# Performance work log

Measured on AMD Instinct MI355X. Metric: run time of the kernel, lower is better.

The kernel has to match this reference:

```python
import jax, jax.numpy as jnp
import numpy as np

N_NODES = 100000
N_EDGES = 3200000
D_FEAT = 256
FILTERS = 256


def setup_inputs() -> dict:
    key = jax.random.key(0)
    k1, k2, k3, k4, k5 = jax.random.split(key, 5)
    x = jax.random.normal(k1, (N_NODES, D_FEAT), dtype=jnp.float32)
    edge_row = jax.random.randint(k2, (N_EDGES,), 0, N_NODES, dtype=jnp.int32)
    edge_col = jax.random.randint(k3, (N_EDGES,), 0, N_NODES, dtype=jnp.int32)
    edge_vals = jnp.ones((N_EDGES,), dtype=jnp.float32)
    w = jax.random.normal(k4, (D_FEAT, FILTERS), dtype=jnp.float32) * (2.0 / D_FEAT) ** 0.5  # he_normal
    b = jax.random.normal(k5, (FILTERS,), dtype=jnp.float32) * 0.05
    return {"x": x, "edge_row": edge_row, "edge_col": edge_col,
            "edge_vals": edge_vals, "w": w, "b": b}


def reference(x, edge_row, edge_col, edge_vals, w, b):
    n = x.shape[0]
    # normalize_A: D = rowsum(A); L = D^{-1/2} A D^{-1/2}
    deg = jax.ops.segment_sum(edge_vals, edge_row, num_segments=n)
    dinv = jnp.where(deg > 0, deg ** -0.5, 0.0)  # [N]
    norm_vals = edge_vals * dinv[edge_row] * dinv[edge_col]  # [E]
    # dense projection then sparse aggregation + bias + relu
    h = x @ w  # [N, F]
    msg = norm_vals[:, None] * h[edge_col]  # [E, F] gather + scale
    agg = jax.ops.segment_sum(msg, edge_row, num_segments=n)  # [N, F]
    return jax.nn.relu(agg + b)
```

## Files before the change

kernel.cpp:

```cpp
#include <hip/hip_runtime.h>
#include <hip/hip_bf16.h>


#define DF   256
#define RSH  7
#define RPB  128
#define CAP  4800
#define CHUNK 8192

typedef __attribute__((ext_vector_type(8))) short short8;
typedef __attribute__((ext_vector_type(4))) float f32x4;

__device__ __forceinline__ unsigned short f2bf(float f) {
    unsigned int u = __float_as_uint(f);
    unsigned int r = (u + 0x7fffu + ((u >> 16) & 1u)) >> 16;
    return (unsigned short)r;
}
__device__ __forceinline__ unsigned int pack2(float a, float b) {
    return (unsigned)f2bf(a) | ((unsigned)f2bf(b) << 16);
}
__device__ __forceinline__ float bflo(unsigned int u) { return __uint_as_float(u << 16); }
__device__ __forceinline__ float bfhi(unsigned int u) { return __uint_as_float(u & 0xffff0000u); }

__global__ __launch_bounds__(256) void bhist_kernel(const int* __restrict__ row,
                                                    int* __restrict__ blockhist, int NB, int E) {
    __shared__ int hist[1024];
    int t = threadIdx.x;
    for (int i = t; i < NB; i += 256) hist[i] = 0;
    __syncthreads();
    int base = blockIdx.x * CHUNK;
    int end = base + CHUNK; if (end > E) end = E;
    for (int i = base + t; i < end; i += 256)
        atomicAdd(&hist[row[i] >> RSH], 1);
    __syncthreads();
    for (int i = t; i < NB; i += 256)
        blockhist[(size_t)blockIdx.x * NB + i] = hist[i];
}

__global__ __launch_bounds__(256) void bscan_kernel(int* __restrict__ blockhist,
                                                    int* __restrict__ buckettot, int NB, int NBLK) {
    __shared__ int ps[256];
    int b = blockIdx.x, t = threadIdx.x;
    int e0 = 2 * t, e1 = 2 * t + 1;
    int v0 = (e0 < NBLK) ? blockhist[(size_t)e0 * NB + b] : 0;
    int v1 = (e1 < NBLK) ? blockhist[(size_t)e1 * NB + b] : 0;
    int tsum = v0 + v1;
    ps[t] = tsum;
    __syncthreads();
    for (int off = 1; off < 256; off <<= 1) {
        int v = (t >= off) ? ps[t - off] : 0;
        __syncthreads();
        ps[t] += v;
        __syncthreads();
    }
    int pre = ps[t] - tsum;
    if (e0 < NBLK) blockhist[(size_t)e0 * NB + b] = pre;
    if (e1 < NBLK) blockhist[(size_t)e1 * NB + b] = pre + v0;
    if (t == 255) buckettot[b] = ps[255];
}

__global__ __launch_bounds__(1024) void btot_kernel(const int* __restrict__ buckettot,
                                                    int* __restrict__ bucket_base, int NB) {
    __shared__ int ps[1024];
    int t = threadIdx.x;
    int v = (t < NB) ? buckettot[t] : 0;
    ps[t] = v;
    __syncthreads();
    for (int off = 1; off < 1024; off <<= 1) {
        int u = (t >= off) ? ps[t - off] : 0;
        __syncthreads();
        ps[t] += u;
        __syncthreads();
    }
    if (t < NB) bucket_base[t] = ps[t] - v;
    if (t == 1023) bucket_base[NB] = ps[1023];
}

__global__ __launch_bounds__(256) void bscatter_kernel(const int* __restrict__ row,
                                                       const int* __restrict__ col,
                                                       const float* __restrict__ vals,
                                                       const int* __restrict__ blockhist,
                                                       const int* __restrict__ bucket_base,
                                                       int2* __restrict__ bedge, int NB, int E) {
    __shared__ int loff[1024];
    int t = threadIdx.x, blk = blockIdx.x;
    for (int i = t; i < NB; i += 256)
        loff[i] = bucket_base[i] + blockhist[(size_t)blk * NB + i];
    __syncthreads();
    int base = blk * CHUNK;
    int end = base + CHUNK; if (end > E) end = E;
    for (int i = base + t; i < end; i += 256) {
        int r = row[i];
        int p = atomicAdd(&loff[r >> RSH], 1);
        bedge[p] = make_int2(((r & (RPB - 1)) << 17) | col[i], __float_as_int(vals[i]));
    }
}

__global__ __launch_bounds__(256) void deg_kernel(const int2* __restrict__ bedge,
                                                  const int* __restrict__ bucket_base,
                                                  float* __restrict__ dinv, int N) {
    __shared__ float acc[RPB];
    int b = blockIdx.x, t = threadIdx.x;
    if (t < RPB) acc[t] = 0.f;
    __syncthreads();
    int s = bucket_base[b], e = bucket_base[b + 1];
    for (int i = s + t; i < e; i += 256) {
        int2 ed = bedge[i];
        atomicAdd(&acc[ed.x >> 17], __int_as_float(ed.y));
    }
    __syncthreads();
    if (t < RPB) {
        int r = b * RPB + t;
        if (r < N) {
            float d = acc[t];
            dinv[r] = (d > 0.f) ? (1.0f / sqrtf(d)) : 0.f;
        }
    }
}

__global__ __launch_bounds__(256) void transpose_kernel(const float* __restrict__ w,
                                                        float* __restrict__ wT) {
    __shared__ float tile[32][33];
    int bx = blockIdx.x * 32, by = blockIdx.y * 32;
    int tx = threadIdx.x, ty = threadIdx.y;
    for (int j = ty; j < 32; j += 8) tile[j][tx] = w[(by + j) * DF + bx + tx];
    __syncthreads();
    for (int j = ty; j < 32; j += 8) wT[(bx + j) * DF + by + tx] = tile[tx][j];
}

__global__ __launch_bounds__(256) void gemm_kernel(const float* __restrict__ x,
                                                   const float* __restrict__ wT,
                                                   const float* __restrict__ dinv,
                                                   unsigned short* __restrict__ h, int N) {
    __shared__ unsigned short Al[128 * 32];
    __shared__ unsigned short Bl[128 * 32];
    int tid = threadIdx.x;
    int by = blockIdx.x, bx = blockIdx.y;
    int wv = tid >> 6, lane = tid & 63;
    int wr = wv >> 1, wc = wv & 1;
    int q = lane >> 4, mi = lane & 15;

    f32x4 acc[4][4];
#pragma unroll
    for (int i = 0; i < 4; ++i)
#pragma unroll
        for (int j = 0; j < 4; ++j) acc[i][j] = (f32x4){0.f, 0.f, 0.f, 0.f};

    int srow = tid >> 1;
    int sseg = (tid & 1) * 16;
    int axrow = by * 128 + srow; if (axrow >= N) axrow = N - 1;
    const float* ax = x + (long)axrow * DF + sseg;
    const float* bxp = wT + (long)(bx * 128 + srow) * DF + sseg;
    unsigned short* Aw = &Al[srow * 32 + sseg];
    unsigned short* Bw = &Bl[srow * 32 + sseg];

    for (int kk = 0; kk < DF; kk += 32) {
        float4 a0 = *(const float4*)(ax + kk);
        float4 a1 = *(const float4*)(ax + kk + 4);
        float4 a2 = *(const float4*)(ax + kk + 8);
        float4 a3 = *(const float4*)(ax + kk + 12);
        float4 b0 = *(const float4*)(bxp + kk);
        float4 b1 = *(const float4*)(bxp + kk + 4);
        float4 b2 = *(const float4*)(bxp + kk + 8);
        float4 b3 = *(const float4*)(bxp + kk + 12);
        __syncthreads();
        uint4 pa, pb;
        pa.x = pack2(a0.x, a0.y); pa.y = pack2(a0.z, a0.w);
        pa.z = pack2(a1.x, a1.y); pa.w = pack2(a1.z, a1.w);
        *(uint4*)Aw = pa;
        pa.x = pack2(a2.x, a2.y); pa.y = pack2(a2.z, a2.w);
        pa.z = pack2(a3.x, a3.y); pa.w = pack2(a3.z, a3.w);
        *(uint4*)(Aw + 8) = pa;
        pb.x = pack2(b0.x, b0.y); pb.y = pack2(b0.z, b0.w);
        pb.z = pack2(b1.x, b1.y); pb.w = pack2(b1.z, b1.w);
        *(uint4*)Bw = pb;
        pb.x = pack2(b2.x, b2.y); pb.y = pack2(b2.z, b2.w);
        pb.z = pack2(b3.x, b3.y); pb.w = pack2(b3.z, b3.w);
        *(uint4*)(Bw + 8) = pb;
        __syncthreads();

        short8 af[4], bf[4];
#pragma unroll
        for (int i = 0; i < 4; ++i)
            af[i] = *(const short8*)&Al[(wr * 64 + i * 16 + mi) * 32 + q * 8];
#pragma unroll
        for (int j = 0; j < 4; ++j)
            bf[j] = *(const short8*)&Bl[(wc * 64 + j * 16 + mi) * 32 + q * 8];
#pragma unroll
        for (int i = 0; i < 4; ++i)
#pragma unroll
            for (int j = 0; j < 4; ++j)
                acc[i][j] = __builtin_amdgcn_mfma_f32_16x16x32_bf16(af[i], bf[j], acc[i][j], 0, 0, 0);
    }

#pragma unroll
    for (int i = 0; i < 4; ++i) {
        int base_row = by * 128 + wr * 64 + i * 16 + q * 4;
#pragma unroll
        for (int r = 0; r < 4; ++r) {
            int rg = base_row + r;
            if (rg < N) {
                float dv = dinv[rg];
#pragma unroll
                for (int j = 0; j < 4; ++j) {
                    int cg = bx * 128 + wc * 64 + j * 16 + mi;
                    h[(long)rg * DF + cg] = f2bf(dv * acc[i][j][r]);
                }
            }
        }
    }
}

__global__ __launch_bounds__(256) void aggb_kernel(const unsigned short* __restrict__ h,
                                                   const int2* __restrict__ bedge,
                                                   const int* __restrict__ bucket_base,
                                                   const float* __restrict__ dinv,
                                                   const float* __restrict__ bias,
                                                   float* __restrict__ out, int N) {
    __shared__ int2 ledge[CAP];
    __shared__ int cnt[RPB];
    __shared__ int lrs[RPB + 1];
    __shared__ int lfill[RPB];
    int b = blockIdx.x, t = threadIdx.x;
    int s = bucket_base[b], e = bucket_base[b + 1];
    int tot = e - s;
    int cap_end = s + (tot < CAP ? tot : CAP);
    if (t < RPB) { cnt[t] = 0; lfill[t] = 0; }
    __syncthreads();
    for (int i = s + t; i < cap_end; i += 256)
        atomicAdd(&cnt[bedge[i].x >> 17], 1);
    __syncthreads();
    int myc = 0;
    if (t < RPB) { myc = cnt[t]; lrs[t] = myc; }
    __syncthreads();
    for (int off = 1; off < RPB; off <<= 1) {
        int v = (t < RPB && t >= off) ? lrs[t - off] : 0;
        __syncthreads();
        if (t < RPB) lrs[t] += v;
        __syncthreads();
    }
    if (t < RPB) {
        int iv = lrs[t];
        lrs[t] = iv - myc;
        if (t == RPB - 1) lrs[RPB] = iv;
    }
    __syncthreads();
    for (int i = s + t; i < cap_end; i += 256) {
        int2 ed = bedge[i];
        int rl = ed.x >> 17;
        int p = lrs[rl] + atomicAdd(&lfill[rl], 1);
        ledge[p] = make_int2(ed.x & 0x1FFFF, ed.y);
    }
    __syncthreads();
    int wv = t >> 6, lane = t & 63;
    int half = lane >> 5;
    int fl = (lane & 31) * 8;
    const unsigned short* hp = h + fl;
    for (int lr = wv; lr < RPB; lr += 4) {
        int r = b * RPB + lr;
        if (r >= N) break;
        int rs = lrs[lr], re = lrs[lr + 1];
        float a0 = 0, a1 = 0, a2 = 0, a3 = 0, a4 = 0, a5 = 0, a6 = 0, a7 = 0;
        int i = rs + half;
        for (; i + 6 < re; i += 8) {
            int2 e0 = ledge[i], e1 = ledge[i + 2], e2 = ledge[i + 4], e3 = ledge[i + 6];
            uint4 u0 = *(const uint4*)(hp + (long)e0.x * DF);
            uint4 u1 = *(const uint4*)(hp + (long)e1.x * DF);
            uint4 u2 = *(const uint4*)(hp + (long)e2.x * DF);
            uint4 u3 = *(const uint4*)(hp + (long)e3.x * DF);
            float v0 = __int_as_float(e0.y), v1 = __int_as_float(e1.y);
            float v2 = __int_as_float(e2.y), v3 = __int_as_float(e3.y);
            a0 += v0 * bflo(u0.x) + v1 * bflo(u1.x) + v2 * bflo(u2.x) + v3 * bflo(u3.x);
            a1 += v0 * bfhi(u0.x) + v1 * bfhi(u1.x) + v2 * bfhi(u2.x) + v3 * bfhi(u3.x);
            a2 += v0 * bflo(u0.y) + v1 * bflo(u1.y) + v2 * bflo(u2.y) + v3 * bflo(u3.y);
            a3 += v0 * bfhi(u0.y) + v1 * bfhi(u1.y) + v2 * bfhi(u2.y) + v3 * bfhi(u3.y);
            a4 += v0 * bflo(u0.z) + v1 * bflo(u1.z) + v2 * bflo(u2.z) + v3 * bflo(u3.z);
            a5 += v0 * bfhi(u0.z) + v1 * bfhi(u1.z) + v2 * bfhi(u2.z) + v3 * bfhi(u3.z);
            a6 += v0 * bflo(u0.w) + v1 * bflo(u1.w) + v2 * bflo(u2.w) + v3 * bflo(u3.w);
            a7 += v0 * bfhi(u0.w) + v1 * bfhi(u1.w) + v2 * bfhi(u2.w) + v3 * bfhi(u3.w);
        }
        for (; i < re; i += 2) {
            int2 e0 = ledge[i];
            float v0 = __int_as_float(e0.y);
            uint4 u0 = *(const uint4*)(hp + (long)e0.x * DF);
            a0 += v0 * bflo(u0.x); a1 += v0 * bfhi(u0.x);
            a2 += v0 * bflo(u0.y); a3 += v0 * bfhi(u0.y);
            a4 += v0 * bflo(u0.z); a5 += v0 * bfhi(u0.z);
            a6 += v0 * bflo(u0.w); a7 += v0 * bfhi(u0.w);
        }
        for (int j = cap_end + half; j < e; j += 2) {
            int2 ed = bedge[j];
            if ((ed.x >> 17) == lr) {
                float v0 = __int_as_float(ed.y);
                uint4 u0 = *(const uint4*)(hp + (long)(ed.x & 0x1FFFF) * DF);
                a0 += v0 * bflo(u0.x); a1 += v0 * bfhi(u0.x);
                a2 += v0 * bflo(u0.y); a3 += v0 * bfhi(u0.y);
                a4 += v0 * bflo(u0.z); a5 += v0 * bfhi(u0.z);
                a6 += v0 * bflo(u0.w); a7 += v0 * bfhi(u0.w);
            }
        }
        a0 += __shfl_xor(a0, 32); a1 += __shfl_xor(a1, 32);
        a2 += __shfl_xor(a2, 32); a3 += __shfl_xor(a3, 32);
        a4 += __shfl_xor(a4, 32); a5 += __shfl_xor(a5, 32);
        a6 += __shfl_xor(a6, 32); a7 += __shfl_xor(a7, 32);
        if (half == 0) {
            float dr = dinv[r];
            float4 b0 = *(const float4*)(bias + fl);
            float4 b1 = *(const float4*)(bias + fl + 4);
            float4 o0, o1;
            o0.x = fmaxf(fmaf(dr, a0, b0.x), 0.f);
            o0.y = fmaxf(fmaf(dr, a1, b0.y), 0.f);
            o0.z = fmaxf(fmaf(dr, a2, b0.z), 0.f);
            o0.w = fmaxf(fmaf(dr, a3, b0.w), 0.f);
            o1.x = fmaxf(fmaf(dr, a4, b1.x), 0.f);
            o1.y = fmaxf(fmaf(dr, a5, b1.y), 0.f);
            o1.z = fmaxf(fmaf(dr, a6, b1.z), 0.f);
            o1.w = fmaxf(fmaf(dr, a7, b1.w), 0.f);
            *(float4*)(out + (long)r * DF + fl) = o0;
            *(float4*)(out + (long)r * DF + fl + 4) = o1;
        }
    }
}

extern "C" void kernel_launch(void* const* d_in, const int* in_sizes, int n_in,
                              void* d_out, int out_size, void* d_ws, size_t ws_size,
                              hipStream_t stream) {
    const float* x   = (const float*)d_in[0];
    const int* erow  = (const int*)d_in[1];
    const int* ecol  = (const int*)d_in[2];
    const float* ev  = (const float*)d_in[3];
    const float* w   = (const float*)d_in[4];
    const float* b   = (const float*)d_in[5];
    float* out = (float*)d_out;

    int N = in_sizes[0] / DF;
    int E = in_sizes[1];
    int NB = (N + RPB - 1) >> RSH;
    int NBLK = (E + CHUNK - 1) / CHUNK;

    char* ws = (char*)d_ws;
    size_t Ea8 = (((size_t)E * 8) + 255) & ~(size_t)255;
    size_t Hs  = (((size_t)N * DF * 2) + 255) & ~(size_t)255;
    size_t Na  = (((size_t)N * 4) + 255) & ~(size_t)255;

    int2* bedge = (int2*)ws;
    char* reg2 = ws + Ea8;
    unsigned short* h = (unsigned short*)reg2;
    int* blockhist = (int*)reg2;
    char* reg3 = reg2 + Hs;
    float* wT = (float*)reg3;
    float* dinv = (float*)(reg3 + 262144);
    int* buckettot = (int*)(reg3 + 262144 + Na);
    int* bucket_base = (int*)(reg3 + 262144 + Na + 8192);

    bhist_kernel<<<NBLK, 256, 0, stream>>>(erow, blockhist, NB, E);
    bscan_kernel<<<NB, 256, 0, stream>>>(blockhist, buckettot, NB, NBLK);
    btot_kernel<<<1, 1024, 0, stream>>>(buckettot, bucket_base, NB);
    bscatter_kernel<<<NBLK, 256, 0, stream>>>(erow, ecol, ev, blockhist, bucket_base, bedge, NB, E);
    deg_kernel<<<NB, 256, 0, stream>>>(bedge, bucket_base, dinv, N);
    transpose_kernel<<<dim3(8, 8), dim3(32, 8), 0, stream>>>(w, wT);
    gemm_kernel<<<dim3((N + 127) / 128, DF / 128), 256, 0, stream>>>(x, wT, dinv, h, N);
    aggb_kernel<<<NB, 256, 0, stream>>>(h, bedge, bucket_base, dinv, b, out, N);
}
```

Measured before the change: 595.0 us.

## Sort edges by row in degree pass, widen GEMM tile, transpose block histogram

The degree kernel becomes a resort kernel. It counts and sums edges per row, then writes each bucket's edges back in row-sorted order, so the aggregation kernel only binary-searches row starts instead of redoing the counting sort. The GEMM now computes all 256 output columns per block, which drops the second grid column and halves re-reading of x. It also pads the LDS stride to reduce bank conflicts and sets an occupancy hint. The block histogram is stored transposed so the scan reads coalesced, at the cost of a second histogram buffer, more GEMM registers and an extra global write pass over the edges.

```diff
diff --git a/kernel.cpp b/kernel.cpp
--- a/kernel.cpp
+++ b/kernel.cpp
@@ -7,6 +7,7 @@
 #define RPB  128
 #define CAP  4800
 #define CHUNK 8192
+#define LSTR 40
 
 typedef __attribute__((ext_vector_type(8))) short short8;
 typedef __attribute__((ext_vector_type(4))) float f32x4;
@@ -23,7 +24,7 @@
 __device__ __forceinline__ float bfhi(unsigned int u) { return __uint_as_float(u & 0xffff0000u); }
 
 __global__ __launch_bounds__(256) void bhist_kernel(const int* __restrict__ row,
-                                                    int* __restrict__ blockhist, int NB, int E) {
+                                                    int* __restrict__ bh1, int NB, int NBLK, int E) {
     __shared__ int hist[1024];
     int t = threadIdx.x;
     for (int i = t; i < NB; i += 256) hist[i] = 0;
@@ -34,16 +35,17 @@
         atomicAdd(&hist[row[i] >> RSH], 1);
     __syncthreads();
     for (int i = t; i < NB; i += 256)
-        blockhist[(size_t)blockIdx.x * NB + i] = hist[i];
-}
-
-__global__ __launch_bounds__(256) void bscan_kernel(int* __restrict__ blockhist,
+        bh1[(size_t)i * NBLK + blockIdx.x] = hist[i];
+}
+
+__global__ __launch_bounds__(256) void bscan_kernel(const int* __restrict__ bh1,
+                                                    int* __restrict__ bh2,
                                                     int* __restrict__ buckettot, int NB, int NBLK) {
     __shared__ int ps[256];
     int b = blockIdx.x, t = threadIdx.x;
     int e0 = 2 * t, e1 = 2 * t + 1;
-    int v0 = (e0 < NBLK) ? blockhist[(size_t)e0 * NB + b] : 0;
-    int v1 = (e1 < NBLK) ? blockhist[(size_t)e1 * NB + b] : 0;
+    int v0 = (e0 < NBLK) ? bh1[(size_t)b * NBLK + e0] : 0;
+    int v1 = (e1 < NBLK) ? bh1[(size_t)b * NBLK + e1] : 0;
     int tsum = v0 + v1;
     ps[t] = tsum;
     __syncthreads();
@@ -54,8 +56,8 @@
         __syncthreads();
     }
     int pre = ps[t] - tsum;
-    if (e0 < NBLK) blockhist[(size_t)e0 * NB + b] = pre;
-    if (e1 < NBLK) blockhist[(size_t)e1 * NB + b] = pre + v0;
+    if (e0 < NBLK) bh2[(size_t)e0 * NB + b] = pre;
+    if (e1 < NBLK) bh2[(size_t)e1 * NB + b] = pre + v0;
     if (t == 255) buckettot[b] = ps[255];
 }
 
@@ -79,13 +81,13 @@
 __global__ __launch_bounds__(256) void bscatter_kernel(const int* __restrict__ row,
                                                        const int* __restrict__ col,
                                                        const float* __restrict__ vals,
-                                                       const int* __restrict__ blockhist,
+                                                       const int* __restrict__ bh2,
                                                        const int* __restrict__ bucket_base,
                                                        int2* __restrict__ bedge, int NB, int E) {
     __shared__ int loff[1024];
     int t = threadIdx.x, blk = blockIdx.x;
     for (int i = t; i < NB; i += 256)
-        loff[i] = bucket_base[i] + blockhist[(size_t)blk * NB + i];
+        loff[i] = bucket_base[i] + bh2[(size_t)blk * NB + i];
     __syncthreads();
     int base = blk * CHUNK;
     int end = base + CHUNK; if (end > E) end = E;
@@ -96,25 +98,69 @@
     }
 }
 
-__global__ __launch_bounds__(256) void deg_kernel(const int2* __restrict__ bedge,
-                                                  const int* __restrict__ bucket_base,
-                                                  float* __restrict__ dinv, int N) {
-    __shared__ float acc[RPB];
+__global__ __launch_bounds__(256) void resort_kernel(int2* __restrict__ bedge,
+                                                     const int* __restrict__ bucket_base,
+                                                     float* __restrict__ dinv, int N) {
+    __shared__ int2 ledge[CAP];
+    __shared__ int cnt[RPB];
+    __shared__ float facc[RPB];
+    __shared__ int lrs[RPB];
+    __shared__ int lfill[RPB];
     int b = blockIdx.x, t = threadIdx.x;
-    if (t < RPB) acc[t] = 0.f;
-    __syncthreads();
     int s = bucket_base[b], e = bucket_base[b + 1];
-    for (int i = s + t; i < e; i += 256) {
-        int2 ed = bedge[i];
-        atomicAdd(&acc[ed.x >> 17], __int_as_float(ed.y));
-    }
-    __syncthreads();
+    int tot = e - s;
+    int ncap = tot < CAP ? tot : CAP;
+    if (t < RPB) { cnt[t] = 0; facc[t] = 0.f; lfill[t] = 0; }
+    for (int i = t; i < ncap; i += 256) ledge[i] = bedge[s + i];
+    int2 ov[8]; int nov = 0;
+#pragma unroll
+    for (int k = 0; k < 8; ++k) {
+        int idx = CAP + t + k * 256;
+        if (idx < tot) { ov[k] = bedge[s + idx]; nov = k + 1; }
+    }
+    __syncthreads();
+    for (int i = t; i < ncap; i += 256) {
+        int2 ed = ledge[i];
+        int rl = ed.x >> 17;
+        atomicAdd(&cnt[rl], 1);
+        atomicAdd(&facc[rl], __int_as_float(ed.y));
+    }
+#pragma unroll
+    for (int k = 0; k < 8; ++k) if (k < nov) {
+        int rl = ov[k].x >> 17;
+        atomicAdd(&cnt[rl], 1);
+        atomicAdd(&facc[rl], __int_as_float(ov[k].y));
+    }
+    __syncthreads();
+    int myc = 0;
+    if (t < RPB) { myc = cnt[t]; lrs[t] = myc; }
+    __syncthreads();
+    for (int off = 1; off < RPB; off <<= 1) {
+        int v = (t < RPB && t >= off) ? lrs[t - off] : 0;
+        __syncthreads();
+        if (t < RPB) lrs[t] += v;
+        __syncthreads();
+    }
+    if (t < RPB) lrs[t] -= myc;
     if (t < RPB) {
         int r = b * RPB + t;
         if (r < N) {
-            float d = acc[t];
+            float d = facc[t];
             dinv[r] = (d > 0.f) ? (1.0f / sqrtf(d)) : 0.f;
         }
+    }
+    __syncthreads();
+    for (int i = t; i < ncap; i += 256) {
+        int2 ed = ledge[i];
+        int rl = ed.x >> 17;
+        int p = atomicAdd(&lfill[rl], 1);
+        bedge[s + lrs[rl] + p] = ed;
+    }
+#pragma unroll
+    for (int k = 0; k < 8; ++k) if (k < nov) {
+        int rl = ov[k].x >> 17;
+        int p = atomicAdd(&lfill[rl], 1);
+        bedge[s + lrs[rl] + p] = ov[k];
     }
 }
 
@@ -128,31 +174,31 @@
     for (int j = ty; j < 32; j += 8) wT[(bx + j) * DF + by + tx] = tile[tx][j];
 }
 
-__global__ __launch_bounds__(256) void gemm_kernel(const float* __restrict__ x,
-                                                   const float* __restrict__ wT,
-                                                   const float* __restrict__ dinv,
-                                                   unsigned short* __restrict__ h, int N) {
-    __shared__ unsigned short Al[128 * 32];
-    __shared__ unsigned short Bl[128 * 32];
+__global__ __launch_bounds__(256, 2) void gemm_kernel(const float* __restrict__ x,
+                                                      const float* __restrict__ wT,
+                                                      const float* __restrict__ dinv,
+                                                      unsigned short* __restrict__ h, int N) {
+    __shared__ unsigned short Al[128 * LSTR];
+    __shared__ unsigned short Bl[256 * LSTR];
     int tid = threadIdx.x;
-    int by = blockIdx.x, bx = blockIdx.y;
+    int by = blockIdx.x;
     int wv = tid >> 6, lane = tid & 63;
     int wr = wv >> 1, wc = wv & 1;
     int q = lane >> 4, mi = lane & 15;
 
-    f32x4 acc[4][4];
+    f32x4 acc[4][8];
 #pragma unroll
     for (int i = 0; i < 4; ++i)
 #pragma unroll
-        for (int j = 0; j < 4; ++j) acc[i][j] = (f32x4){0.f, 0.f, 0.f, 0.f};
+        for (int j = 0; j < 8; ++j) acc[i][j] = (f32x4){0.f, 0.f, 0.f, 0.f};
 
     int srow = tid >> 1;
     int sseg = (tid & 1) * 16;
     int axrow = by * 128 + srow; if (axrow >= N) axrow = N - 1;
     const float* ax = x + (long)axrow * DF + sseg;
-    const float* bxp = wT + (long)(bx * 128 + srow) * DF + sseg;
-    unsigned short* Aw = &Al[srow * 32 + sseg];
-    unsigned short* Bw = &Bl[srow * 32 + sseg];
+    const float* bxp = wT + (long)tid * DF;
+    unsigned short* Aw = &Al[srow * LSTR + sseg];
+    unsigned short* Bw = &Bl[tid * LSTR];
 
     for (int kk = 0; kk < DF; kk += 32) {
         float4 a0 = *(const float4*)(ax + kk);
@@ -163,34 +209,44 @@
         float4 b1 = *(const float4*)(bxp + kk + 4);
         float4 b2 = *(const float4*)(bxp + kk + 8);
         float4 b3 = *(const float4*)(bxp + kk + 12);
-        __syncthreads();
-        uint4 pa, pb;
+        float4 b4 = *(const float4*)(bxp + kk + 16);
+        float4 b5 = *(const float4*)(bxp + kk + 20);
+        float4 b6 = *(const float4*)(bxp + kk + 24);
+        float4 b7 = *(const float4*)(bxp + kk + 28);
+        __syncthreads();
+        uint4 pa;
         pa.x = pack2(a0.x, a0.y); pa.y = pack2(a0.z, a0.w);
         pa.z = pack2(a1.x, a1.y); pa.w = pack2(a1.z, a1.w);
         *(uint4*)Aw = pa;
         pa.x = pack2(a2.x, a2.y); pa.y = pack2(a2.z, a2.w);
         pa.z = pack2(a3.x, a3.y); pa.w = pack2(a3.z, a3.w);
         *(uint4*)(Aw + 8) = pa;
+        uint4 pb;
         pb.x = pack2(b0.x, b0.y); pb.y = pack2(b0.z, b0.w);
         pb.z = pack2(b1.x, b1.y); pb.w = pack2(b1.z, b1.w);
         *(uint4*)Bw = pb;
         pb.x = pack2(b2.x, b2.y); pb.y = pack2(b2.z, b2.w);
         pb.z = pack2(b3.x, b3.y); pb.w = pack2(b3.z, b3.w);
         *(uint4*)(Bw + 8) = pb;
-        __syncthreads();
-
-        short8 af[4], bf[4];
+        pb.x = pack2(b4.x, b4.y); pb.y = pack2(b4.z, b4.w);
+        pb.z = pack2(b5.x, b5.y); pb.w = pack2(b5.z, b5.w);
+        *(uint4*)(Bw + 16) = pb;
+        pb.x = pack2(b6.x, b6.y); pb.y = pack2(b6.z, b6.w);
+        pb.z = pack2(b7.x, b7.y); pb.w = pack2(b7.z, b7.w);
+        *(uint4*)(Bw + 24) = pb;
+        __syncthreads();
+
+        short8 af[4];
 #pragma unroll
         for (int i = 0; i < 4; ++i)
-            af[i] = *(const short8*)&Al[(wr * 64 + i * 16 + mi) * 32 + q * 8];
-#pragma unroll
-        for (int j = 0; j < 4; ++j)
-            bf[j] = *(const short8*)&Bl[(wc * 64 + j * 16 + mi) * 32 + q * 8];
-#pragma unroll
-        for (int i = 0; i < 4; ++i)
-#pragma unroll
-            for (int j = 0; j < 4; ++j)
-                acc[i][j] = __builtin_amdgcn_mfma_f32_16x16x32_bf16(af[i], bf[j], acc[i][j], 0, 0, 0);
+            af[i] = *(const short8*)&Al[(wr * 64 + i * 16 + mi) * LSTR + q * 8];
+#pragma unroll
+        for (int j = 0; j < 8; ++j) {
+            short8 bfj = *(const short8*)&Bl[(wc * 128 + j * 16 + mi) * LSTR + q * 8];
+#pragma unroll
+            for (int i = 0; i < 4; ++i)
+                acc[i][j] = __builtin_amdgcn_mfma_f32_16x16x32_bf16(af[i], bfj, acc[i][j], 0, 0, 0);
+        }
     }
 
 #pragma unroll
@@ -202,8 +258,8 @@
             if (rg < N) {
                 float dv = dinv[rg];
 #pragma unroll
-                for (int j = 0; j < 4; ++j) {
-                    int cg = bx * 128 + wc * 64 + j * 16 + mi;
+                for (int j = 0; j < 8; ++j) {
+                    int cg = wc * 128 + j * 16 + mi;
                     h[(long)rg * DF + cg] = f2bf(dv * acc[i][j][r]);
                 }
             }
@@ -218,38 +274,20 @@
                                                    const float* __restrict__ bias,
                                                    float* __restrict__ out, int N) {
     __shared__ int2 ledge[CAP];
-    __shared__ int cnt[RPB];
     __shared__ int lrs[RPB + 1];
-    __shared__ int lfill[RPB];
     int b = blockIdx.x, t = threadIdx.x;
     int s = bucket_base[b], e = bucket_base[b + 1];
     int tot = e - s;
-    int cap_end = s + (tot < CAP ? tot : CAP);
-    if (t < RPB) { cnt[t] = 0; lfill[t] = 0; }
-    __syncthreads();
-    for (int i = s + t; i < cap_end; i += 256)
-        atomicAdd(&cnt[bedge[i].x >> 17], 1);
-    __syncthreads();
-    int myc = 0;
-    if (t < RPB) { myc = cnt[t]; lrs[t] = myc; }
-    __syncthreads();
-    for (int off = 1; off < RPB; off <<= 1) {
-        int v = (t < RPB && t >= off) ? lrs[t - off] : 0;
-        __syncthreads();
-        if (t < RPB) lrs[t] += v;
-        __syncthreads();
-    }
-    if (t < RPB) {
-        int iv = lrs[t];
-        lrs[t] = iv - myc;
-        if (t == RPB - 1) lrs[RPB] = iv;
-    }
-    __syncthreads();
-    for (int i = s + t; i < cap_end; i += 256) {
-        int2 ed = bedge[i];
-        int rl = ed.x >> 17;
-        int p = lrs[rl] + atomicAdd(&lfill[rl], 1);
-        ledge[p] = make_int2(ed.x & 0x1FFFF, ed.y);
+    int ncap = tot < CAP ? tot : CAP;
+    for (int i = t; i < ncap; i += 256) ledge[i] = bedge[s + i];
+    __syncthreads();
+    if (t < RPB + 1) {
+        int lo = 0, hi = ncap;
+        while (lo < hi) {
+            int m = (lo + hi) >> 1;
+            if ((ledge[m].x >> 17) < t) lo = m + 1; else hi = m;
+        }
+        lrs[t] = lo;
     }
     __syncthreads();
     int wv = t >> 6, lane = t & 63;
@@ -264,10 +302,10 @@
         int i = rs + half;
         for (; i + 6 < re; i += 8) {
             int2 e0 = ledge[i], e1 = ledge[i + 2], e2 = ledge[i + 4], e3 = ledge[i + 6];
-            uint4 u0 = *(const uint4*)(hp + (long)e0.x * DF);
-            uint4 u1 = *(const uint4*)(hp + (long)e1.x * DF);
-            uint4 u2 = *(const uint4*)(hp + (long)e2.x * DF);
-            uint4 u3 = *(const uint4*)(hp + (long)e3.x * DF);
+            uint4 u0 = *(const uint4*)(hp + (long)(e0.x & 0x1FFFF) * DF);
+            uint4 u1 = *(const uint4*)(hp + (long)(e1.x & 0x1FFFF) * DF);
+            uint4 u2 = *(const uint4*)(hp + (long)(e2.x & 0x1FFFF) * DF);
+            uint4 u3 = *(const uint4*)(hp + (long)(e3.x & 0x1FFFF) * DF);
             float v0 = __int_as_float(e0.y), v1 = __int_as_float(e1.y);
             float v2 = __int_as_float(e2.y), v3 = __int_as_float(e3.y);
             a0 += v0 * bflo(u0.x) + v1 * bflo(u1.x) + v2 * bflo(u2.x) + v3 * bflo(u3.x);
@@ -279,18 +317,19 @@
             a6 += v0 * bflo(u0.w) + v1 * bflo(u1.w) + v2 * bflo(u2.w) + v3 * bflo(u3.w);
             a7 += v0 * bfhi(u0.w) + v1 * bfhi(u1.w) + v2 * bfhi(u2.w) + v3 * bfhi(u3.w);
         }
-        for (; i < re; i += 2) {
+        for (; i < re && i < ncap; i += 2) {
             int2 e0 = ledge[i];
             float v0 = __int_as_float(e0.y);
-            uint4 u0 = *(const uint4*)(hp + (long)e0.x * DF);
+            uint4 u0 = *(const uint4*)(hp + (long)(e0.x & 0x1FFFF) * DF);
             a0 += v0 * bflo(u0.x); a1 += v0 * bfhi(u0.x);
             a2 += v0 * bflo(u0.y); a3 += v0 * bfhi(u0.y);
             a4 += v0 * bflo(u0.z); a5 += v0 * bfhi(u0.z);
             a6 += v0 * bflo(u0.w); a7 += v0 * bfhi(u0.w);
         }
-        for (int j = cap_end + half; j < e; j += 2) {
-            int2 ed = bedge[j];
-            if ((ed.x >> 17) == lr) {
+        if (tot > CAP && re > CAP) {
+            int j2 = (rs > CAP ? rs : CAP) + half;
+            for (; j2 < re; j2 += 2) {
+                int2 ed = bedge[s + j2];
                 float v0 = __int_as_float(ed.y);
                 uint4 u0 = *(const uint4*)(hp + (long)(ed.x & 0x1FFFF) * DF);
                 a0 += v0 * bflo(u0.x); a1 += v0 * bfhi(u0.x);
@@ -346,19 +385,20 @@
     int2* bedge = (int2*)ws;
     char* reg2 = ws + Ea8;
     unsigned short* h = (unsigned short*)reg2;
-    int* blockhist = (int*)reg2;
+    int* bh1 = (int*)reg2;
+    int* bh2 = bh1 + (size_t)NB * NBLK;
     char* reg3 = reg2 + Hs;
     float* wT = (float*)reg3;
     float* dinv = (float*)(reg3 + 262144);
     int* buckettot = (int*)(reg3 + 262144 + Na);
     int* bucket_base = (int*)(reg3 + 262144 + Na + 8192);
 
-    bhist_kernel<<<NBLK, 256, 0, stream>>>(erow, blockhist, NB, E);
-    bscan_kernel<<<NB, 256, 0, stream>>>(blockhist, buckettot, NB, NBLK);
+    bhist_kernel<<<NBLK, 256, 0, stream>>>(erow, bh1, NB, NBLK, E);
+    bscan_kernel<<<NB, 256, 0, stream>>>(bh1, bh2, buckettot, NB, NBLK);
     btot_kernel<<<1, 1024, 0, stream>>>(buckettot, bucket_base, NB);
-    bscatter_kernel<<<NBLK, 256, 0, stream>>>(erow, ecol, ev, blockhist, bucket_base, bedge, NB, E);
-    deg_kernel<<<NB, 256, 0, stream>>>(bedge, bucket_base, dinv, N);
+    bscatter_kernel<<<NBLK, 256, 0, stream>>>(erow, ecol, ev, bh2, bucket_base, bedge, NB, E);
+    resort_kernel<<<NB, 256, 0, stream>>>(bedge, bucket_base, dinv, N);
     transpose_kernel<<<dim3(8, 8), dim3(32, 8), 0, stream>>>(w, wT);
-    gemm_kernel<<<dim3((N + 127) / 128, DF / 128), 256, 0, stream>>>(x, wT, dinv, h, N);
+    gemm_kernel<<<dim3((N + 127) / 128), 256, 0, stream>>>(x, wT, dinv, h, N);
     aggb_kernel<<<NB, 256, 0, stream>>>(h, bedge, bucket_base, dinv, b, out, N);
 }
```

After: 617.6 us. 3.8% more time.
